# Optimization experiments

Hardware: AMD Instinct MI355X
Metric: run time of the kernel (lower is better)

Reference implementation:

```python
import jax, jax.numpy as jnp
import numpy as np

H = 256

def setup_inputs() -> dict:
    key = jax.random.key(0)
    ks = jax.random.split(key, 9)
    s = 1.0 / np.sqrt(H)
    x = jax.random.normal(ks[0], (8, 2048, H), dtype=jnp.float32)
    Wq = jax.random.uniform(ks[1], (H, H), jnp.float32, -s, s)
    bq = jax.random.uniform(ks[2], (H,), jnp.float32, -s, s)
    Wk = jax.random.uniform(ks[3], (H, H), jnp.float32, -s, s)
    bk = jax.random.uniform(ks[4], (H,), jnp.float32, -s, s)
    Wv = jax.random.uniform(ks[5], (H, H), jnp.float32, -s, s)
    bv = jax.random.uniform(ks[6], (H,), jnp.float32, -s, s)
    Ww = jax.random.uniform(ks[7], (H, 1), jnp.float32, -s, s)
    bw = jax.random.uniform(ks[8], (1,), jnp.float32, -s, s)
    return {"x": x, "Wq": Wq, "bq": bq, "Wk": Wk, "bk": bk,
            "Wv": Wv, "bv": bv, "Ww": Ww, "bw": bw}

def reference(x, Wq, bq, Wk, bk, Wv, bv, Ww, bw):
    # x: (B, N, H) — cross-asset attention over N assets
    q = x @ Wq + bq
    k = x @ Wk + bk
    v = x @ Wv + bv
    scale = 1.0 / jnp.sqrt(jnp.asarray(q.shape[-1], q.dtype))
    beta = jnp.einsum('bnd,bmd->bnm', q, k) * scale  # (B, N, N)
    beta = jax.nn.softmax(beta, axis=-1)
    # original: sum(value[:,None] * beta[...,None], dim=2) == beta @ v
    out = jnp.einsum('bnm,bmd->bnd', beta, v)
    final_scores = (out @ Ww + bw)[..., 0]  # (B, N)
    return final_scores
```

## Files before the change

kernel.cpp:

```cpp
#include <hip/hip_runtime.h>

#define H 256
#define NB 2048
#define BATCH 8
#define NSPLIT 8
#define KSPAN (NB / NSPLIT)
#define NITER (KSPAN / 64)

typedef unsigned short u16;
using bf16x8 = __attribute__((ext_vector_type(8))) __bf16;
using f32x4  = __attribute__((ext_vector_type(4))) float;

typedef const __attribute__((address_space(1))) void gv_t;
typedef __attribute__((address_space(3))) void lv_t;

__device__ __forceinline__ void gl_lds16(const void* g, void* l) {
    __builtin_amdgcn_global_load_lds((gv_t*)g, (lv_t*)l, 16, 0, 0);
}

#define MFMA(a, b, c) __builtin_amdgcn_mfma_f32_16x16x32_bf16(a, b, c, 0, 0, 0)

__device__ __forceinline__ u16 f2bf(float f) {
    union { float f; unsigned u; } v; v.f = f;
    unsigned r = v.u + 0x7fffu + ((v.u >> 16) & 1u);
    return (u16)(r >> 16);
}

__device__ __forceinline__ bf16x8 cvt8(const float* p) {
    float4 f0 = *(const float4*)p;
    float4 f1 = *(const float4*)(p + 4);
    union { bf16x8 v; u16 u[8]; } r;
    r.u[0] = f2bf(f0.x); r.u[1] = f2bf(f0.y); r.u[2] = f2bf(f0.z); r.u[3] = f2bf(f0.w);
    r.u[4] = f2bf(f1.x); r.u[5] = f2bf(f1.y); r.u[6] = f2bf(f1.z); r.u[7] = f2bf(f1.w);
    return r.v;
}

__global__ __launch_bounds__(256) void prep_kernel(
        const float* __restrict__ Wq, const float* __restrict__ Wk,
        const float* __restrict__ Wv, const float* __restrict__ Ww,
        const float* __restrict__ bq, const float* __restrict__ bv,
        u16* __restrict__ aTb, float* __restrict__ wvw,
        float* __restrict__ kbv, float* __restrict__ ccp) {
    __shared__ u16 bt[16384];
    int id = blockIdx.x, t = threadIdx.x;

    if (id < 256) {
        int f = id;
        float p = Wv[f * H + t] * Ww[t];
        float r = Wk[f * H + t] * bq[t];
        float c = (id == 0) ? bv[t] * Ww[t] : 0.f;
        for (int o = 32; o; o >>= 1) {
            p += __shfl_xor(p, o); r += __shfl_xor(r, o); c += __shfl_xor(c, o);
        }
        __shared__ float redp[4], redr[4], redc[4];
        int w = t >> 6, lane = t & 63;
        if (lane == 0) { redp[w] = p; redr[w] = r; redc[w] = c; }
        __syncthreads();
        if (t == 0) {
            wvw[f] = redp[0] + redp[1] + redp[2] + redp[3];
            kbv[f] = redr[0] + redr[1] + redr[2] + redr[3];
            if (f == 0) ccp[0] = redc[0] + redc[1] + redc[2] + redc[3];
        }
        return;
    }

    int gid = id - 256;
    int mb = (gid >> 2) * 128, nb = (gid & 3) * 64;
    int w = t >> 6, lane = t & 63, l15 = lane & 15, quad = lane >> 4;

    {
        const float* src = Wq + (nb + w * 16 + l15) * H + quad * 8;
        #pragma unroll
        for (int ks = 0; ks < 8; ++ks)
            *(bf16x8*)(bt + (w * 8 + ks) * 512 + lane * 8) = cvt8(src + ks * 32);
    }

    bf16x8 a[2][8];
    #pragma unroll
    for (int mi = 0; mi < 2; ++mi) {
        const float* ab = Wk + (mb + w * 32 + mi * 16 + l15) * H + quad * 8;
        #pragma unroll
        for (int ks = 0; ks < 8; ++ks) a[mi][ks] = cvt8(ab + ks * 32);
    }
    __syncthreads();

    f32x4 acc[2][4] = {};
    #pragma unroll
    for (int ks = 0; ks < 8; ++ks)
        #pragma unroll
        for (int tt = 0; tt < 4; ++tt) {
            bf16x8 b = *(const bf16x8*)(bt + ((tt * 8 + ks) * 64 + lane) * 8);
            acc[0][tt] = MFMA(a[0][ks], b, acc[0][tt]);
            acc[1][tt] = MFMA(a[1][ks], b, acc[1][tt]);
        }

    #pragma unroll
    for (int mi = 0; mi < 2; ++mi) {
        int m = mb + w * 32 + mi * 16 + quad * 4;
        #pragma unroll
        for (int tt = 0; tt < 4; ++tt) {
            int n = nb + tt * 16 + l15;
            #pragma unroll
            for (int r2 = 0; r2 < 4; ++r2)
                aTb[(m + r2) * H + n] = f2bf(acc[mi][tt][r2] * 0.0625f);
        }
    }
}

__global__ __launch_bounds__(256) void xt_kernel(
        const float* __restrict__ x, const u16* __restrict__ aTb,
        const float* __restrict__ wvw, const float* __restrict__ kbv,
        const float* __restrict__ ccp,
        u16* __restrict__ xbf, float2* __restrict__ uee, u16* __restrict__ Tbf) {
    __shared__ u16 bt[16384];
    int id = blockIdx.x, tid = threadIdx.x;
    int nbI = (id >> 3) & 3;
    int mb4 = (id & 7) + (id >> 5) * 8;
    int mb = mb4 * 128, nb = nbI * 64;
    int w = tid >> 6, lane = tid & 63, l15 = lane & 15, quad = lane >> 4;

    {
        const u16* gsrc = aTb + (nb + w * 16 + l15) * H + quad * 8;
        #pragma unroll
        for (int ks = 0; ks < 8; ++ks)
            gl_lds16(gsrc + ks * 32, bt + (w * 8 + ks) * 512);
    }

    bf16x8 a[2][8];
    float s[2] = {0.f, 0.f}, d[2] = {0.f, 0.f};
    #pragma unroll
    for (int ks = 0; ks < 8; ++ks) {
        const float* wp = wvw + ks * 32 + quad * 8;
        const float* kp = kbv + ks * 32 + quad * 8;
        float4 w0 = *(const float4*)wp, w1 = *(const float4*)(wp + 4);
        float4 k0 = *(const float4*)kp, k1 = *(const float4*)(kp + 4);
        #pragma unroll
        for (int mi = 0; mi < 2; ++mi) {
            const float* xr = x + (size_t)(mb + w * 32 + mi * 16 + l15) * H + ks * 32 + quad * 8;
            float4 f0 = *(const float4*)xr;
            float4 f1 = *(const float4*)(xr + 4);
            union { bf16x8 v; u16 u[8]; } r;
            r.u[0] = f2bf(f0.x); r.u[1] = f2bf(f0.y); r.u[2] = f2bf(f0.z); r.u[3] = f2bf(f0.w);
            r.u[4] = f2bf(f1.x); r.u[5] = f2bf(f1.y); r.u[6] = f2bf(f1.z); r.u[7] = f2bf(f1.w);
            a[mi][ks] = r.v;
            s[mi] += f0.x * w0.x + f0.y * w0.y + f0.z * w0.z + f0.w * w0.w
                   + f1.x * w1.x + f1.y * w1.y + f1.z * w1.z + f1.w * w1.w;
            d[mi] += f0.x * k0.x + f0.y * k0.y + f0.z * k0.z + f0.w * k0.w
                   + f1.x * k1.x + f1.y * k1.y + f1.z * k1.z + f1.w * k1.w;
        }
    }

    if (nbI == 0) {
        #pragma unroll
        for (int mi = 0; mi < 2; ++mi) {
            u16* xo = xbf + (size_t)(mb + w * 32 + mi * 16 + l15) * H + quad * 8;
            #pragma unroll
            for (int ks = 0; ks < 8; ++ks)
                *(bf16x8*)(xo + ks * 32) = a[mi][ks];
        }
        float cc = ccp[0];
        #pragma unroll
        for (int mi = 0; mi < 2; ++mi) {
            float ss = s[mi] + __shfl_xor(s[mi], 16);
            ss += __shfl_xor(ss, 32);
            float dd = d[mi] + __shfl_xor(d[mi], 16);
            dd += __shfl_xor(dd, 32);
            if (quad == 0) {
                int row = mb + w * 32 + mi * 16 + l15;
                float e = __expf(dd * 0.0625f);
                uee[row] = make_float2(e * (ss + cc), e);
            }
        }
    }
    __syncthreads();

    f32x4 acc[2][4] = {};
    #pragma unroll
    for (int ks = 0; ks < 8; ++ks)
        #pragma unroll
        for (int tt = 0; tt < 4; ++tt) {
            bf16x8 b = *(const bf16x8*)(bt + ((tt * 8 + ks) * 64 + lane) * 8);
            acc[0][tt] = MFMA(a[0][ks], b, acc[0][tt]);
            acc[1][tt] = MFMA(a[1][ks], b, acc[1][tt]);
        }

    #pragma unroll
    for (int mi = 0; mi < 2; ++mi) {
        int m = mb + w * 32 + mi * 16 + quad * 4;
        #pragma unroll
        for (int tt = 0; tt < 4; ++tt) {
            int n = nb + tt * 16 + l15;
            #pragma unroll
            for (int r2 = 0; r2 < 4; ++r2)
                Tbf[(size_t)(m + r2) * H + n] = f2bf(acc[mi][tt][r2]);
        }
    }
}

__global__ __launch_bounds__(256, 2) void attn_kernel(
        const u16* __restrict__ T, const u16* __restrict__ xbf,
        const float2* __restrict__ uee,
        float* __restrict__ pnum, float* __restrict__ pden) {
    __shared__ u16 kt[32768];
    int tid = threadIdx.x;
    int id = blockIdx.x;
    int b = id & 7, rest = id >> 3;
    int qc = rest & 7, sp = rest >> 3;
    int w = tid >> 6, lane = tid & 63, l15 = lane & 15, quad = lane >> 4;
    int qb = qc * 256;

    bf16x8 aq[4][8];
    {
        const u16* qbase = T + (size_t)(b * NB + qb + w * 64 + l15) * H + quad * 8;
        #pragma unroll
        for (int mi = 0; mi < 4; ++mi)
            #pragma unroll
            for (int ks = 0; ks < 8; ++ks)
                aq[mi][ks] = *(const bf16x8*)(qbase + mi * 16 * H + ks * 32);
    }

    const u16* xb = xbf + (size_t)b * NB * H;
    const float2* uep = uee + (size_t)b * NB;
    const int kb0 = sp * KSPAN;

    const u16* gsrc = xb + (size_t)(kb0 + w * 16 + l15) * H + quad * 8;
    #pragma unroll
    for (int j = 0; j < 8; ++j)
        gl_lds16(gsrc + j * 32, kt + (w * 8 + j) * 512);
    __syncthreads();

    float ls[4][4] = {}, as_[4][4] = {};

    #pragma unroll 1
    for (int h = 0; h < NITER; ++h) {
        const u16* ktc = kt + (h & 1) * 16384;
        if (h + 1 < NITER) {
            u16* dst = kt + ((h & 1) ^ 1) * 16384;
            const u16* g2 = gsrc + (size_t)(h + 1) * 64 * H;
            #pragma unroll
            for (int j = 0; j < 8; ++j)
                gl_lds16(g2 + j * 32, dst + (w * 8 + j) * 512);
        }
        int kb64 = kb0 + h * 64;
        float2 uv[4];
        #pragma unroll
        for (int t = 0; t < 4; ++t) uv[t] = uep[kb64 + t * 16 + l15];

        #pragma unroll
        for (int t = 0; t < 4; ++t) {
            f32x4 acc[4] = {};
            __builtin_amdgcn_s_setprio(1);
            #pragma unroll
            for (int ks = 0; ks < 8; ++ks) {
                bf16x8 bfr = *(const bf16x8*)(ktc + ((t * 8 + ks) * 64 + lane) * 8);
                acc[0] = MFMA(aq[0][ks], bfr, acc[0]);
                acc[1] = MFMA(aq[1][ks], bfr, acc[1]);
                acc[2] = MFMA(aq[2][ks], bfr, acc[2]);
                acc[3] = MFMA(aq[3][ks], bfr, acc[3]);
            }
            __builtin_amdgcn_s_setprio(0);
            #pragma unroll
            for (int mi = 0; mi < 4; ++mi)
                #pragma unroll
                for (int r = 0; r < 4; ++r) {
                    float p = __expf(acc[mi][r]);
                    as_[mi][r] += p * uv[t].x;
                    ls[mi][r]  += p * uv[t].y;
                }
        }
        __syncthreads();
    }

    #pragma unroll
    for (int mi = 0; mi < 4; ++mi)
        #pragma unroll
        for (int r = 0; r < 4; ++r)
            for (int o = 1; o < 16; o <<= 1) {
                ls[mi][r]  += __shfl_xor(ls[mi][r], o);
                as_[mi][r] += __shfl_xor(as_[mi][r], o);
            }

    if (l15 == 0) {
        size_t base = (size_t)(sp * BATCH + b) * NB + qb + w * 64 + quad * 4;
        #pragma unroll
        for (int mi = 0; mi < 4; ++mi)
            #pragma unroll
            for (int r = 0; r < 4; ++r) {
                pnum[base + mi * 16 + r] = as_[mi][r];
                pden[base + mi * 16 + r] = ls[mi][r];
            }
    }
}

__global__ __launch_bounds__(256) void finalize_kernel(
        const float* __restrict__ pnum, const float* __restrict__ pden,
        const float* __restrict__ bw, float* __restrict__ out) {
    int i = blockIdx.x * 256 + threadIdx.x;
    float num = 0.f, den = 0.f;
    for (int sp = 0; sp < NSPLIT; ++sp) {
        num += pnum[sp * (BATCH * NB) + i];
        den += pden[sp * (BATCH * NB) + i];
    }
    out[i] = num / den + bw[0];
}

extern "C" void kernel_launch(void* const* d_in, const int* in_sizes, int n_in,
                              void* d_out, int out_size, void* d_ws, size_t ws_size,
                              hipStream_t stream) {
    (void)in_sizes; (void)n_in; (void)out_size; (void)ws_size;
    const float* x  = (const float*)d_in[0];
    const float* Wq = (const float*)d_in[1];
    const float* bq = (const float*)d_in[2];
    const float* Wk = (const float*)d_in[3];
    const float* bk = (const float*)d_in[4];  (void)bk;
    const float* Wv = (const float*)d_in[5];
    const float* bv = (const float*)d_in[6];
    const float* Ww = (const float*)d_in[7];
    const float* bw = (const float*)d_in[8];
    float* out = (float*)d_out;

    u16* xbf = (u16*)d_ws;
    u16* Tbf = xbf + 4194304;
    u16* aTb = Tbf + 4194304;
    float* wvw = (float*)(aTb + 65536);
    float* kbv = wvw + 256;
    float* ccp = kbv + 256;
    float2* uee = (float2*)(ccp + 4);
    float* pnum = (float*)(uee + 16384);
    float* pden = pnum + NSPLIT * BATCH * NB;

    hipLaunchKernelGGL(prep_kernel, dim3(264), dim3(256), 0, stream,
                       Wq, Wk, Wv, Ww, bq, bv, aTb, wvw, kbv, ccp);
    hipLaunchKernelGGL(xt_kernel, dim3(512), dim3(256), 0, stream,
                       x, aTb, wvw, kbv, ccp, xbf, uee, Tbf);
    hipLaunchKernelGGL(attn_kernel, dim3(8 * 8 * NSPLIT), dim3(256), 0, stream,
                       Tbf, xbf, uee, pnum, pden);
    hipLaunchKernelGGL(finalize_kernel, dim3(64), dim3(256), 0, stream,
                       pnum, pden, bw, out);
}
```

Before: 133.1 us.

## Fuse finalize into attention via completion counter and restructure xt GEMM per row-block

Removes the separate finalize kernel. The last attention block to finish for each (batch, query-chunk) now sums the split partials and writes the output; it finds out it is last through an atomic counter that prep_kernel zeroes. The xt kernel is also reorganised so each block owns 32 rows across all 256 output columns. Each wave reads its B fragments straight from global memory instead of staging them in LDS behind a barrier. The trade-offs are an extra atomic and threadfence per attention block, and all four waves converting the same x rows redundantly.

```diff
diff --git a/kernel.cpp b/kernel.cpp
--- a/kernel.cpp
+++ b/kernel.cpp
@@ -40,12 +40,13 @@
         const float* __restrict__ Wv, const float* __restrict__ Ww,
         const float* __restrict__ bq, const float* __restrict__ bv,
         u16* __restrict__ aTb, float* __restrict__ wvw,
-        float* __restrict__ kbv, float* __restrict__ ccp) {
+        float* __restrict__ kbv, float* __restrict__ ccp, int* __restrict__ cnt) {
     __shared__ u16 bt[16384];
     int id = blockIdx.x, t = threadIdx.x;
 
     if (id < 256) {
         int f = id;
+        if (id == 0 && t < 64) cnt[t] = 0;
         float p = Wv[f * H + t] * Ww[t];
         float r = Wk[f * H + t] * bq[t];
         float c = (id == 0) ? bv[t] * Ww[t] : 0.f;
@@ -112,19 +113,9 @@
         const float* __restrict__ wvw, const float* __restrict__ kbv,
         const float* __restrict__ ccp,
         u16* __restrict__ xbf, float2* __restrict__ uee, u16* __restrict__ Tbf) {
-    __shared__ u16 bt[16384];
     int id = blockIdx.x, tid = threadIdx.x;
-    int nbI = (id >> 3) & 3;
-    int mb4 = (id & 7) + (id >> 5) * 8;
-    int mb = mb4 * 128, nb = nbI * 64;
     int w = tid >> 6, lane = tid & 63, l15 = lane & 15, quad = lane >> 4;
-
-    {
-        const u16* gsrc = aTb + (nb + w * 16 + l15) * H + quad * 8;
-        #pragma unroll
-        for (int ks = 0; ks < 8; ++ks)
-            gl_lds16(gsrc + ks * 32, bt + (w * 8 + ks) * 512);
-    }
+    int rb = id * 32;
 
     bf16x8 a[2][8];
     float s[2] = {0.f, 0.f}, d[2] = {0.f, 0.f};
@@ -136,7 +127,7 @@
         float4 k0 = *(const float4*)kp, k1 = *(const float4*)(kp + 4);
         #pragma unroll
         for (int mi = 0; mi < 2; ++mi) {
-            const float* xr = x + (size_t)(mb + w * 32 + mi * 16 + l15) * H + ks * 32 + quad * 8;
+            const float* xr = x + (size_t)(rb + mi * 16 + l15) * H + ks * 32 + quad * 8;
             float4 f0 = *(const float4*)xr;
             float4 f1 = *(const float4*)(xr + 4);
             union { bf16x8 v; u16 u[8]; } r;
@@ -150,10 +141,10 @@
         }
     }
 
-    if (nbI == 0) {
+    if (w == 0) {
         #pragma unroll
         for (int mi = 0; mi < 2; ++mi) {
-            u16* xo = xbf + (size_t)(mb + w * 32 + mi * 16 + l15) * H + quad * 8;
+            u16* xo = xbf + (size_t)(rb + mi * 16 + l15) * H + quad * 8;
             #pragma unroll
             for (int ks = 0; ks < 8; ++ks)
                 *(bf16x8*)(xo + ks * 32) = a[mi][ks];
@@ -161,47 +152,43 @@
         float cc = ccp[0];
         #pragma unroll
         for (int mi = 0; mi < 2; ++mi) {
-            float ss = s[mi] + __shfl_xor(s[mi], 16);
-            ss += __shfl_xor(ss, 32);
-            float dd = d[mi] + __shfl_xor(d[mi], 16);
-            dd += __shfl_xor(dd, 32);
+            float ss = s[mi] + __shfl_xor(s[mi], 16); ss += __shfl_xor(ss, 32);
+            float dd = d[mi] + __shfl_xor(d[mi], 16); dd += __shfl_xor(dd, 32);
             if (quad == 0) {
-                int row = mb + w * 32 + mi * 16 + l15;
                 float e = __expf(dd * 0.0625f);
-                uee[row] = make_float2(e * (ss + cc), e);
+                uee[rb + mi * 16 + l15] = make_float2(e * (ss + cc), e);
             }
         }
     }
-    __syncthreads();
-
-    f32x4 acc[2][4] = {};
-    #pragma unroll
-    for (int ks = 0; ks < 8; ++ks)
-        #pragma unroll
-        for (int tt = 0; tt < 4; ++tt) {
-            bf16x8 b = *(const bf16x8*)(bt + ((tt * 8 + ks) * 64 + lane) * 8);
-            acc[0][tt] = MFMA(a[0][ks], b, acc[0][tt]);
-            acc[1][tt] = MFMA(a[1][ks], b, acc[1][tt]);
-        }
-
-    #pragma unroll
-    for (int mi = 0; mi < 2; ++mi) {
-        int m = mb + w * 32 + mi * 16 + quad * 4;
-        #pragma unroll
-        for (int tt = 0; tt < 4; ++tt) {
-            int n = nb + tt * 16 + l15;
-            #pragma unroll
-            for (int r2 = 0; r2 < 4; ++r2)
-                Tbf[(size_t)(m + r2) * H + n] = f2bf(acc[mi][tt][r2]);
+
+    #pragma unroll 1
+    for (int t = 0; t < 4; ++t) {
+        int n = (w * 4 + t) * 16 + l15;
+        const u16* bb = aTb + n * H + quad * 8;
+        bf16x8 bfr[8];
+        #pragma unroll
+        for (int ks = 0; ks < 8; ++ks) bfr[ks] = *(const bf16x8*)(bb + ks * 32);
+        f32x4 acc0 = {}, acc1 = {};
+        #pragma unroll
+        for (int ks = 0; ks < 8; ++ks) {
+            acc0 = MFMA(a[0][ks], bfr[ks], acc0);
+            acc1 = MFMA(a[1][ks], bfr[ks], acc1);
+        }
+        #pragma unroll
+        for (int r2 = 0; r2 < 4; ++r2) {
+            Tbf[(size_t)(rb + quad * 4 + r2) * H + n]      = f2bf(acc0[r2]);
+            Tbf[(size_t)(rb + 16 + quad * 4 + r2) * H + n] = f2bf(acc1[r2]);
         }
     }
 }
 
 __global__ __launch_bounds__(256, 2) void attn_kernel(
         const u16* __restrict__ T, const u16* __restrict__ xbf,
-        const float2* __restrict__ uee,
-        float* __restrict__ pnum, float* __restrict__ pden) {
+        const float2* __restrict__ uee, const float* __restrict__ bw,
+        float* __restrict__ pnum, float* __restrict__ pden,
+        int* __restrict__ cnt, float* __restrict__ out) {
     __shared__ u16 kt[32768];
+    __shared__ int lastf;
     int tid = threadIdx.x;
     int id = blockIdx.x;
     int b = id & 7, rest = id >> 3;
@@ -290,18 +277,25 @@
                 pden[base + mi * 16 + r] = ls[mi][r];
             }
     }
-}
-
-__global__ __launch_bounds__(256) void finalize_kernel(
-        const float* __restrict__ pnum, const float* __restrict__ pden,
-        const float* __restrict__ bw, float* __restrict__ out) {
-    int i = blockIdx.x * 256 + threadIdx.x;
-    float num = 0.f, den = 0.f;
-    for (int sp = 0; sp < NSPLIT; ++sp) {
-        num += pnum[sp * (BATCH * NB) + i];
-        den += pden[sp * (BATCH * NB) + i];
-    }
-    out[i] = num / den + bw[0];
+
+    __syncthreads();
+    if (tid == 0) {
+        __threadfence();
+        int old = atomicAdd(cnt + (b * 8 + qc), 1);
+        lastf = (old == NSPLIT - 1) ? 1 : 0;
+    }
+    __syncthreads();
+    if (lastf) {
+        __threadfence();
+        int row = qb + tid;
+        float num = 0.f, den = 0.f;
+        #pragma unroll
+        for (int s2 = 0; s2 < NSPLIT; ++s2) {
+            num += pnum[(size_t)(s2 * BATCH + b) * NB + row];
+            den += pden[(size_t)(s2 * BATCH + b) * NB + row];
+        }
+        out[(size_t)b * NB + row] = num / den + bw[0];
+    }
 }
 
 extern "C" void kernel_launch(void* const* d_in, const int* in_sizes, int n_in,
@@ -328,13 +322,12 @@
     float2* uee = (float2*)(ccp + 4);
     float* pnum = (float*)(uee + 16384);
     float* pden = pnum + NSPLIT * BATCH * NB;
+    int* cnt = (int*)(pden + NSPLIT * BATCH * NB);
 
     hipLaunchKernelGGL(prep_kernel, dim3(264), dim3(256), 0, stream,
-                       Wq, Wk, Wv, Ww, bq, bv, aTb, wvw, kbv, ccp);
+                       Wq, Wk, Wv, Ww, bq, bv, aTb, wvw, kbv, ccp, cnt);
     hipLaunchKernelGGL(xt_kernel, dim3(512), dim3(256), 0, stream,
                        x, aTb, wvw, kbv, ccp, xbf, uee, Tbf);
     hipLaunchKernelGGL(attn_kernel, dim3(8 * 8 * NSPLIT), dim3(256), 0, stream,
-                       Tbf, xbf, uee, pnum, pden);
-    hipLaunchKernelGGL(finalize_kernel, dim3(64), dim3(256), 0, stream,
-                       pnum, pden, bw, out);
-}
+                       Tbf, xbf, uee, bw, pnum, pden, cnt, out);
+}
```

New measurement: 147.2 us. 10.5% more time.
